# Optimization experiments

Hardware: AMD Instinct MI355X
Metric: run time of the kernel (lower is better)

## Reference

```python
import jax, jax.numpy as jnp
import numpy as np

N, C_IN, H, W = 1024, 22, 19, 19
C_TRUNK, HID, NHIST = 384, 128, 5
HIST_START = 9  # channels 9..13 hold move history planes


def setup_inputs() -> dict:
    key = jax.random.key(0)
    ks = jax.random.split(key, 8)
    return {
        "input_spatial": jax.random.uniform(ks[0], (N, C_IN, H, W), dtype=jnp.float32),
        "trunk_out": jax.random.normal(ks[1], (N, C_TRUNK, H, W), dtype=jnp.float32),
        "w_ih": jax.random.normal(ks[2], (4 * HID, C_TRUNK), dtype=jnp.float32) * 0.05,
        "w_hh": jax.random.normal(ks[3], (4 * HID, HID), dtype=jnp.float32) * 0.05,
        "b_ih": jax.random.normal(ks[4], (4 * HID,), dtype=jnp.float32) * 0.05,
        "b_hh": jax.random.normal(ks[5], (4 * HID,), dtype=jnp.float32) * 0.05,
        "w_proj": jax.random.normal(ks[6], (C_TRUNK, HID), dtype=jnp.float32) * 0.05,
        "b_proj": jax.random.normal(ks[7], (C_TRUNK,), dtype=jnp.float32) * 0.05,
    }


def reference(input_spatial, trunk_out, w_ih, w_hh, b_ih, b_hh, w_proj, b_proj):
    n, _, h, w = input_spatial.shape
    c_trunk = trunk_out.shape[1]
    # --- extract_move_coords (vectorized) ---
    planes = input_spatial[:, HIST_START:HIST_START + NHIST]          # N,5,H,W
    flat = planes.reshape(n, NHIST, h * w)                            # N,5,HW
    has_move = flat.sum(axis=-1) > 0.5                                # N,5 bool
    idx = jnp.argmax(flat, axis=-1)                                   # N,5 (== r*W+c; clamp(-1,min=0)==0 handled by mask)
    # --- gather trunk features at move coords, mask missing moves ---
    trunk_flat = trunk_out.reshape(n, c_trunk, h * w)                 # N,Ct,HW
    feats = jnp.take_along_axis(trunk_flat, idx[:, None, :], axis=2)  # N,Ct,5
    feats = feats.transpose(0, 2, 1) * has_move[..., None].astype(trunk_out.dtype)  # N,5,Ct
    seq = feats[:, ::-1, :]                                           # oldest -> newest
    # --- single-layer LSTM (torch gate order: i, f, g, o) ---
    def step(carry, x_t):
        h_t, c_t = carry
        g = x_t @ w_ih.T + h_t @ w_hh.T + b_ih + b_hh                 # N,4H
        i_g, f_g, g_g, o_g = jnp.split(g, 4, axis=-1)
        c_new = jax.nn.sigmoid(f_g) * c_t + jax.nn.sigmoid(i_g) * jnp.tanh(g_g)
        h_new = jax.nn.sigmoid(o_g) * jnp.tanh(c_new)
        return (h_new, c_new), None

    h0 = jnp.zeros((n, HID), dtype=seq.dtype)
    (h_final, _), _ = jax.lax.scan(step, (h0, h0), seq.transpose(1, 0, 2))
    out = h_final @ w_proj.T + b_proj                                 # N,Ct
    return out[:, :, None, None]                                      # N,Ct,1,1
```

## Files before the change

### kernel.cpp

```cpp
#include <hip/hip_runtime.h>
#include <hip/hip_bf16.h>
#include <float.h>

#define N_SAMP   1024
#define C_IN     22
#define HW       361
#define C_TRUNK  384
#define HID      128
#define NHIST    5
#define HIST_START 9
#define NGATE    512

typedef __attribute__((ext_vector_type(8))) short short8v;
typedef __attribute__((ext_vector_type(4))) float float4v;

static __device__ __forceinline__ ushort f2bf(float x) {
  unsigned int b = __float_as_uint(x);
  b += 0x7fffu + ((b >> 16) & 1u);
  return (ushort)(b >> 16);
}
static __device__ __forceinline__ float bf2f(ushort u) {
  return __uint_as_float(((unsigned int)u) << 16);
}

#define WIH_ELEMS   (NGATE * C_TRUNK)
#define WHH_ELEMS   (NGATE * HID)
#define WPROJ_ELEMS (C_TRUNK * HID)

__global__ __launch_bounds__(384) void prep_kernel(
    const float* __restrict__ inp,
    const float* __restrict__ w_ih,
    const float* __restrict__ w_hh,
    const float* __restrict__ w_proj,
    const float* __restrict__ trunk,
    ushort* __restrict__ w_ihb,
    ushort* __restrict__ w_hhb,
    ushort* __restrict__ w_projb,
    ushort* __restrict__ seq)
{
  const int n    = blockIdx.x;
  const int tid  = threadIdx.x;
  const int wave = tid >> 6;
  const int lane = tid & 63;
  __shared__ int   s_idx[NHIST];
  __shared__ float s_mov[NHIST];

  {
    const int g = n * 384 + tid;
    if (g < WIH_ELEMS) {
      w_ihb[g] = f2bf(w_ih[g]);
    } else if (g < WIH_ELEMS + WHH_ELEMS) {
      const int o = g - WIH_ELEMS;
      w_hhb[o] = f2bf(w_hh[o]);
    } else if (g < WIH_ELEMS + WHH_ELEMS + WPROJ_ELEMS) {
      const int o = g - WIH_ELEMS - WHH_ELEMS;
      w_projb[o] = f2bf(w_proj[o]);
    }
  }

  if (wave < NHIST) {
    const float* base = inp + ((size_t)n * C_IN + HIST_START + wave) * HW;
    float v = -FLT_MAX; int vi = 0; float sum = 0.f;
    #pragma unroll
    for (int r = 0; r < 6; ++r) {
      int i = lane + r * 64;
      if (i < HW) {
        float x = base[i];
        sum += x;
        if (x > v) { v = x; vi = i; }
      }
    }
    #pragma unroll
    for (int m = 1; m < 64; m <<= 1) {
      float v2 = __shfl_xor(v, m);
      int   i2 = __shfl_xor(vi, m);
      float s2 = __shfl_xor(sum, m);
      if (v2 > v || (v2 == v && i2 < vi)) { v = v2; vi = i2; }
      sum += s2;
    }
    if (lane == 0) {
      s_idx[wave] = vi;
      s_mov[wave] = (sum > 0.5f) ? 1.f : 0.f;
    }
  }
  __syncthreads();

  if (tid < 192) {
    const int c = tid;
    const int   i0 = s_idx[4], i1 = s_idx[3], i2 = s_idx[2],
                i3 = s_idx[1], i4 = s_idx[0];
    const float m0 = s_mov[4], m1 = s_mov[3], m2 = s_mov[2],
                m3 = s_mov[1], m4 = s_mov[0];

    const float* ta = trunk + ((size_t)n * C_TRUNK + c) * HW;
    const float* tb = ta + (size_t)192 * HW;
    float a0 = ta[i0], a1 = ta[i1], a2 = ta[i2], a3 = ta[i3], a4 = ta[i4];
    float b0 = tb[i0], b1 = tb[i1], b2 = tb[i2], b3 = tb[i3], b4 = tb[i4];

    ushort* so = seq + (size_t)n * NHIST * C_TRUNK + c;
    so[0 * C_TRUNK]       = f2bf(a0 * m0);
    so[1 * C_TRUNK]       = f2bf(a1 * m1);
    so[2 * C_TRUNK]       = f2bf(a2 * m2);
    so[3 * C_TRUNK]       = f2bf(a3 * m3);
    so[4 * C_TRUNK]       = f2bf(a4 * m4);
    so[0 * C_TRUNK + 192] = f2bf(b0 * m0);
    so[1 * C_TRUNK + 192] = f2bf(b1 * m1);
    so[2 * C_TRUNK + 192] = f2bf(b2 * m2);
    so[3 * C_TRUNK + 192] = f2bf(b3 * m3);
    so[4 * C_TRUNK + 192] = f2bf(b4 * m4);
  }
}

__global__ __launch_bounds__(256) void gates_kernel(
    const ushort* __restrict__ seq,
    const ushort* __restrict__ w_ihb,
    const float*  __restrict__ b_ih,
    const float*  __restrict__ b_hh,
    ushort* __restrict__ G)
{
  __shared__ ushort As[64][40];
  __shared__ ushort Bs[64][40];
  const int tid  = threadIdx.x;
  const int wv   = tid >> 6;
  const int lane = tid & 63;
  const int m0 = blockIdx.y * 64;
  const int j0 = blockIdx.x * 64;
  const int row_l = tid >> 2;
  const int koff  = (tid & 3) * 8;

  float4v acc0 = {0.f,0.f,0.f,0.f};
  float4v acc1 = {0.f,0.f,0.f,0.f};
  float4v acc2 = {0.f,0.f,0.f,0.f};
  float4v acc3 = {0.f,0.f,0.f,0.f};

  const int fr = lane & 15;
  const int fk = (lane >> 4) * 8;

  for (int k0 = 0; k0 < C_TRUNK; k0 += 32) {
    *(short8v*)&As[row_l][koff] =
        *(const short8v*)(seq + (size_t)(m0 + row_l) * C_TRUNK + k0 + koff);
    *(short8v*)&Bs[row_l][koff] =
        *(const short8v*)(w_ihb + (size_t)(j0 + row_l) * C_TRUNK + k0 + koff);
    __syncthreads();

    short8v af  = *(const short8v*)&As[wv * 16 + fr][fk];
    short8v bf0 = *(const short8v*)&Bs[ 0 + fr][fk];
    short8v bf1 = *(const short8v*)&Bs[16 + fr][fk];
    short8v bf2 = *(const short8v*)&Bs[32 + fr][fk];
    short8v bf3 = *(const short8v*)&Bs[48 + fr][fk];
    acc0 = __builtin_amdgcn_mfma_f32_16x16x32_bf16(af, bf0, acc0, 0, 0, 0);
    acc1 = __builtin_amdgcn_mfma_f32_16x16x32_bf16(af, bf1, acc1, 0, 0, 0);
    acc2 = __builtin_amdgcn_mfma_f32_16x16x32_bf16(af, bf2, acc2, 0, 0, 0);
    acc3 = __builtin_amdgcn_mfma_f32_16x16x32_bf16(af, bf3, acc3, 0, 0, 0);
    __syncthreads();
  }

  const int rbase = m0 + wv * 16 + (lane >> 4) * 4;
  #pragma unroll
  for (int j = 0; j < 4; ++j) {
    const float4v a = (j == 0) ? acc0 : (j == 1) ? acc1 : (j == 2) ? acc2 : acc3;
    const int cj = j0 + j * 16 + fr;
    const float bsum = b_ih[cj] + b_hh[cj];
    #pragma unroll
    for (int r = 0; r < 4; ++r)
      G[(size_t)(rbase + r) * NGATE + cj] = f2bf(a[r] + bsum);
  }
}

__global__ __launch_bounds__(512, 2) void lstm_kernel(
    const ushort* __restrict__ G,
    const ushort* __restrict__ w_hhb,
    const ushort* __restrict__ w_projb,
    const float*  __restrict__ b_proj,
    float* __restrict__ out)
{
  const int n0   = blockIdx.x * 4;
  const int tid  = threadIdx.x;
  const int wv   = tid >> 6;
  const int lane = tid & 63;
  const int fr   = lane & 15;
  const int fq   = lane >> 4;

  __shared__ ushort hswz[4][64][8];
  __shared__ float  glds[NGATE][4];

  ((ushort4*)hswz)[tid] = make_ushort4(0, 0, 0, 0);

  const int j0w = wv * 64;
  short8v bfrag[4][4];
  #pragma unroll
  for (int f = 0; f < 4; ++f)
    #pragma unroll
    for (int ks = 0; ks < 4; ++ks)
      bfrag[f][ks] = *(const short8v*)(
          w_hhb + (size_t)(j0w + f*16 + fr) * HID + ks*32 + fq*8);

  float4v gpre[NHIST][4];
  #pragma unroll
  for (int t = 0; t < NHIST; ++t)
    #pragma unroll
    for (int f = 0; f < 4; ++f) {
      float4v v = {0.f, 0.f, 0.f, 0.f};
      if (fq == 0) {
        const int col = j0w + f*16 + fr;
        #pragma unroll
        for (int r = 0; r < 4; ++r)
          v[r] = bf2f(G[((size_t)(n0 + r) * NHIST + t) * NGATE + col]);
      }
      gpre[t][f] = v;
    }

  float c4[4] = {0.f, 0.f, 0.f, 0.f};
  __syncthreads();

  #pragma unroll
  for (int t = 0; t < NHIST; ++t) {
    short8v af0 = *(const short8v*)&hswz[0][lane][0];
    short8v af1 = *(const short8v*)&hswz[1][lane][0];
    short8v af2 = *(const short8v*)&hswz[2][lane][0];
    short8v af3 = *(const short8v*)&hswz[3][lane][0];
    #pragma unroll
    for (int f = 0; f < 4; ++f) {
      float4v acc = gpre[t][f];
      acc = __builtin_amdgcn_mfma_f32_16x16x32_bf16(af0, bfrag[f][0], acc, 0, 0, 0);
      acc = __builtin_amdgcn_mfma_f32_16x16x32_bf16(af1, bfrag[f][1], acc, 0, 0, 0);
      acc = __builtin_amdgcn_mfma_f32_16x16x32_bf16(af2, bfrag[f][2], acc, 0, 0, 0);
      acc = __builtin_amdgcn_mfma_f32_16x16x32_bf16(af3, bfrag[f][3], acc, 0, 0, 0);
      if (fq == 0)
        *(float4v*)&glds[j0w + f*16 + fr][0] = acc;
    }
    __syncthreads();

    if (tid < HID) {
      const int j = tid;
      float4 iv = *(const float4*)&glds[      j][0];
      float4 fv = *(const float4*)&glds[128 + j][0];
      float4 gv = *(const float4*)&glds[256 + j][0];
      float4 ov = *(const float4*)&glds[384 + j][0];
      float ia[4] = {iv.x, iv.y, iv.z, iv.w};
      float fa[4] = {fv.x, fv.y, fv.z, fv.w};
      float ga[4] = {gv.x, gv.y, gv.z, gv.w};
      float oa[4] = {ov.x, ov.y, ov.z, ov.w};
      #pragma unroll
      for (int s = 0; s < 4; ++s) {
        float ig = 1.f / (1.f + __expf(-ia[s]));
        float fg = 1.f / (1.f + __expf(-fa[s]));
        float og = 1.f / (1.f + __expf(-oa[s]));
        c4[s] = fg * c4[s] + ig * tanhf(ga[s]);
        float h = og * tanhf(c4[s]);
        hswz[j >> 5][((j >> 3) & 3) * 16 + s][j & 7] = f2bf(h);
      }
    }
    __syncthreads();
  }

  const int j0p = wv * 48;
  short8v pfrag[3][4];
  #pragma unroll
  for (int f = 0; f < 3; ++f)
    #pragma unroll
    for (int ks = 0; ks < 4; ++ks)
      pfrag[f][ks] = *(const short8v*)(
          w_projb + (size_t)(j0p + f*16 + fr) * HID + ks*32 + fq*8);

  short8v hf0 = *(const short8v*)&hswz[0][lane][0];
  short8v hf1 = *(const short8v*)&hswz[1][lane][0];
  short8v hf2 = *(const short8v*)&hswz[2][lane][0];
  short8v hf3 = *(const short8v*)&hswz[3][lane][0];
  #pragma unroll
  for (int f = 0; f < 3; ++f) {
    const int col = j0p + f * 16 + fr;
    const float bp = b_proj[col];
    float4v acc = {bp, bp, bp, bp};
    acc = __builtin_amdgcn_mfma_f32_16x16x32_bf16(hf0, pfrag[f][0], acc, 0, 0, 0);
    acc = __builtin_amdgcn_mfma_f32_16x16x32_bf16(hf1, pfrag[f][1], acc, 0, 0, 0);
    acc = __builtin_amdgcn_mfma_f32_16x16x32_bf16(hf2, pfrag[f][2], acc, 0, 0, 0);
    acc = __builtin_amdgcn_mfma_f32_16x16x32_bf16(hf3, pfrag[f][3], acc, 0, 0, 0);
    if (fq == 0) {
      #pragma unroll
      for (int r = 0; r < 4; ++r)
        out[(size_t)(n0 + r) * C_TRUNK + col] = acc[r];
    }
  }
}

extern "C" void kernel_launch(void* const* d_in, const int* in_sizes, int n_in,
                              void* d_out, int out_size, void* d_ws, size_t ws_size,
                              hipStream_t stream) {
  const float* inp    = (const float*)d_in[0];
  const float* trunk  = (const float*)d_in[1];
  const float* w_ih   = (const float*)d_in[2];
  const float* w_hh   = (const float*)d_in[3];
  const float* b_ih   = (const float*)d_in[4];
  const float* b_hh   = (const float*)d_in[5];
  const float* w_proj = (const float*)d_in[6];
  const float* b_proj = (const float*)d_in[7];
  float* out = (float*)d_out;

  char* ws = (char*)d_ws;
  ushort* w_ihb   = (ushort*)ws;
  ushort* w_hhb   = (ushort*)(ws + 393216);
  ushort* w_projb = (ushort*)(ws + 524288);
  ushort* seq     = (ushort*)(ws + 622592);
  ushort* G       = (ushort*)(ws + 4554752);

  prep_kernel<<<N_SAMP, 384, 0, stream>>>(inp, w_ih, w_hh, w_proj, trunk,
                                          w_ihb, w_hhb, w_projb, seq);
  gates_kernel<<<dim3(NGATE / 64, (N_SAMP * NHIST) / 64), 256, 0, stream>>>(
      seq, w_ihb, b_ih, b_hh, G);
  lstm_kernel<<<N_SAMP / 4, 512, 0, stream>>>(G, w_hhb, w_projb, b_proj, out);
}
```

Measured before the change: 72.12 us.

## Fuse gather, input-gate GEMM and LSTM into one kernel per sample group

Splits weight conversion into its own small kernel, then fuses move extraction, trunk gather, the input-to-hidden GEMM and the LSTM recurrence into one kernel handling 4 samples per block. The gathered sequence stays in LDS and the gate pre-activations stay in registers, so the seq and G global round-trips and one launch go away. The cost is that the input GEMM now runs MFMA tiles with only 4 of 16 rows valid, which wastes matrix throughput. Each block also rereads the full w_ih from cache.

```diff
diff --git a/kernel.cpp b/kernel.cpp
--- a/kernel.cpp
+++ b/kernel.cpp
@@ -19,158 +19,40 @@
   b += 0x7fffu + ((b >> 16) & 1u);
   return (ushort)(b >> 16);
 }
-static __device__ __forceinline__ float bf2f(ushort u) {
-  return __uint_as_float(((unsigned int)u) << 16);
-}
 
 #define WIH_ELEMS   (NGATE * C_TRUNK)
 #define WHH_ELEMS   (NGATE * HID)
 #define WPROJ_ELEMS (C_TRUNK * HID)
-
-__global__ __launch_bounds__(384) void prep_kernel(
-    const float* __restrict__ inp,
+#define TOT_CVT     (WIH_ELEMS + WHH_ELEMS + WPROJ_ELEMS)
+
+__global__ __launch_bounds__(512) void precvt_kernel(
     const float* __restrict__ w_ih,
     const float* __restrict__ w_hh,
     const float* __restrict__ w_proj,
-    const float* __restrict__ trunk,
     ushort* __restrict__ w_ihb,
     ushort* __restrict__ w_hhb,
-    ushort* __restrict__ w_projb,
-    ushort* __restrict__ seq)
+    ushort* __restrict__ w_projb)
 {
-  const int n    = blockIdx.x;
-  const int tid  = threadIdx.x;
-  const int wave = tid >> 6;
-  const int lane = tid & 63;
-  __shared__ int   s_idx[NHIST];
-  __shared__ float s_mov[NHIST];
-
-  {
-    const int g = n * 384 + tid;
-    if (g < WIH_ELEMS) {
-      w_ihb[g] = f2bf(w_ih[g]);
-    } else if (g < WIH_ELEMS + WHH_ELEMS) {
-      const int o = g - WIH_ELEMS;
-      w_hhb[o] = f2bf(w_hh[o]);
-    } else if (g < WIH_ELEMS + WHH_ELEMS + WPROJ_ELEMS) {
-      const int o = g - WIH_ELEMS - WHH_ELEMS;
-      w_projb[o] = f2bf(w_proj[o]);
-    }
-  }
-
-  if (wave < NHIST) {
-    const float* base = inp + ((size_t)n * C_IN + HIST_START + wave) * HW;
-    float v = -FLT_MAX; int vi = 0; float sum = 0.f;
-    #pragma unroll
-    for (int r = 0; r < 6; ++r) {
-      int i = lane + r * 64;
-      if (i < HW) {
-        float x = base[i];
-        sum += x;
-        if (x > v) { v = x; vi = i; }
-      }
-    }
-    #pragma unroll
-    for (int m = 1; m < 64; m <<= 1) {
-      float v2 = __shfl_xor(v, m);
-      int   i2 = __shfl_xor(vi, m);
-      float s2 = __shfl_xor(sum, m);
-      if (v2 > v || (v2 == v && i2 < vi)) { v = v2; vi = i2; }
-      sum += s2;
-    }
-    if (lane == 0) {
-      s_idx[wave] = vi;
-      s_mov[wave] = (sum > 0.5f) ? 1.f : 0.f;
-    }
-  }
-  __syncthreads();
-
-  if (tid < 192) {
-    const int c = tid;
-    const int   i0 = s_idx[4], i1 = s_idx[3], i2 = s_idx[2],
-                i3 = s_idx[1], i4 = s_idx[0];
-    const float m0 = s_mov[4], m1 = s_mov[3], m2 = s_mov[2],
-                m3 = s_mov[1], m4 = s_mov[0];
-
-    const float* ta = trunk + ((size_t)n * C_TRUNK + c) * HW;
-    const float* tb = ta + (size_t)192 * HW;
-    float a0 = ta[i0], a1 = ta[i1], a2 = ta[i2], a3 = ta[i3], a4 = ta[i4];
-    float b0 = tb[i0], b1 = tb[i1], b2 = tb[i2], b3 = tb[i3], b4 = tb[i4];
-
-    ushort* so = seq + (size_t)n * NHIST * C_TRUNK + c;
-    so[0 * C_TRUNK]       = f2bf(a0 * m0);
-    so[1 * C_TRUNK]       = f2bf(a1 * m1);
-    so[2 * C_TRUNK]       = f2bf(a2 * m2);
-    so[3 * C_TRUNK]       = f2bf(a3 * m3);
-    so[4 * C_TRUNK]       = f2bf(a4 * m4);
-    so[0 * C_TRUNK + 192] = f2bf(b0 * m0);
-    so[1 * C_TRUNK + 192] = f2bf(b1 * m1);
-    so[2 * C_TRUNK + 192] = f2bf(b2 * m2);
-    so[3 * C_TRUNK + 192] = f2bf(b3 * m3);
-    so[4 * C_TRUNK + 192] = f2bf(b4 * m4);
-  }
-}
-
-__global__ __launch_bounds__(256) void gates_kernel(
-    const ushort* __restrict__ seq,
+  const int g = blockIdx.x * 512 + threadIdx.x;
+  if (g < WIH_ELEMS) {
+    w_ihb[g] = f2bf(w_ih[g]);
+  } else if (g < WIH_ELEMS + WHH_ELEMS) {
+    const int o = g - WIH_ELEMS;
+    w_hhb[o] = f2bf(w_hh[o]);
+  } else if (g < TOT_CVT) {
+    const int o = g - WIH_ELEMS - WHH_ELEMS;
+    w_projb[o] = f2bf(w_proj[o]);
+  }
+}
+
+__global__ __launch_bounds__(512) void mega_kernel(
+    const float*  __restrict__ inp,
+    const float*  __restrict__ trunk,
     const ushort* __restrict__ w_ihb,
+    const ushort* __restrict__ w_hhb,
+    const ushort* __restrict__ w_projb,
     const float*  __restrict__ b_ih,
     const float*  __restrict__ b_hh,
-    ushort* __restrict__ G)
-{
-  __shared__ ushort As[64][40];
-  __shared__ ushort Bs[64][40];
-  const int tid  = threadIdx.x;
-  const int wv   = tid >> 6;
-  const int lane = tid & 63;
-  const int m0 = blockIdx.y * 64;
-  const int j0 = blockIdx.x * 64;
-  const int row_l = tid >> 2;
-  const int koff  = (tid & 3) * 8;
-
-  float4v acc0 = {0.f,0.f,0.f,0.f};
-  float4v acc1 = {0.f,0.f,0.f,0.f};
-  float4v acc2 = {0.f,0.f,0.f,0.f};
-  float4v acc3 = {0.f,0.f,0.f,0.f};
-
-  const int fr = lane & 15;
-  const int fk = (lane >> 4) * 8;
-
-  for (int k0 = 0; k0 < C_TRUNK; k0 += 32) {
-    *(short8v*)&As[row_l][koff] =
-        *(const short8v*)(seq + (size_t)(m0 + row_l) * C_TRUNK + k0 + koff);
-    *(short8v*)&Bs[row_l][koff] =
-        *(const short8v*)(w_ihb + (size_t)(j0 + row_l) * C_TRUNK + k0 + koff);
-    __syncthreads();
-
-    short8v af  = *(const short8v*)&As[wv * 16 + fr][fk];
-    short8v bf0 = *(const short8v*)&Bs[ 0 + fr][fk];
-    short8v bf1 = *(const short8v*)&Bs[16 + fr][fk];
-    short8v bf2 = *(const short8v*)&Bs[32 + fr][fk];
-    short8v bf3 = *(const short8v*)&Bs[48 + fr][fk];
-    acc0 = __builtin_amdgcn_mfma_f32_16x16x32_bf16(af, bf0, acc0, 0, 0, 0);
-    acc1 = __builtin_amdgcn_mfma_f32_16x16x32_bf16(af, bf1, acc1, 0, 0, 0);
-    acc2 = __builtin_amdgcn_mfma_f32_16x16x32_bf16(af, bf2, acc2, 0, 0, 0);
-    acc3 = __builtin_amdgcn_mfma_f32_16x16x32_bf16(af, bf3, acc3, 0, 0, 0);
-    __syncthreads();
-  }
-
-  const int rbase = m0 + wv * 16 + (lane >> 4) * 4;
-  #pragma unroll
-  for (int j = 0; j < 4; ++j) {
-    const float4v a = (j == 0) ? acc0 : (j == 1) ? acc1 : (j == 2) ? acc2 : acc3;
-    const int cj = j0 + j * 16 + fr;
-    const float bsum = b_ih[cj] + b_hh[cj];
-    #pragma unroll
-    for (int r = 0; r < 4; ++r)
-      G[(size_t)(rbase + r) * NGATE + cj] = f2bf(a[r] + bsum);
-  }
-}
-
-__global__ __launch_bounds__(512, 2) void lstm_kernel(
-    const ushort* __restrict__ G,
-    const ushort* __restrict__ w_hhb,
-    const ushort* __restrict__ w_projb,
     const float*  __restrict__ b_proj,
     float* __restrict__ out)
 {
@@ -181,37 +63,101 @@
   const int fr   = lane & 15;
   const int fq   = lane >> 4;
 
+  __shared__ int    s_idx[4][NHIST];
+  __shared__ float  s_mov[4][NHIST];
+  __shared__ ushort seqs[4][NHIST][392];
   __shared__ ushort hswz[4][64][8];
   __shared__ float  glds[NGATE][4];
 
   ((ushort4*)hswz)[tid] = make_ushort4(0, 0, 0, 0);
 
+  for (int task = wv; task < 4 * NHIST; task += 8) {
+    const int s = task / NHIST, p = task - s * NHIST;
+    const float* base = inp + ((size_t)(n0 + s) * C_IN + HIST_START + p) * HW;
+    float v = -FLT_MAX; int vi = 0; float sum = 0.f;
+    #pragma unroll
+    for (int r6 = 0; r6 < 6; ++r6) {
+      int i = lane + r6 * 64;
+      if (i < HW) {
+        float x = base[i];
+        sum += x;
+        if (x > v) { v = x; vi = i; }
+      }
+    }
+    #pragma unroll
+    for (int m = 1; m < 64; m <<= 1) {
+      float v2 = __shfl_xor(v, m);
+      int   i2 = __shfl_xor(vi, m);
+      float s2 = __shfl_xor(sum, m);
+      if (v2 > v || (v2 == v && i2 < vi)) { v = v2; vi = i2; }
+      sum += s2;
+    }
+    if (lane == 0) {
+      s_idx[s][p] = vi;
+      s_mov[s][p] = (sum > 0.5f) ? 1.f : 0.f;
+    }
+  }
+  __syncthreads();
+
+  {
+    const int r0 = tid, r1 = tid + 512, r2 = tid + 1024;
+    const int sa = r0 / C_TRUNK, ca = r0 - sa * C_TRUNK;
+    const int sb = r1 / C_TRUNK, cb = r1 - sb * C_TRUNK;
+    const int sc = r2 / C_TRUNK, cc = r2 - sc * C_TRUNK;
+    const float* ta = trunk + ((size_t)(n0 + sa) * C_TRUNK + ca) * HW;
+    const float* tb = trunk + ((size_t)(n0 + sb) * C_TRUNK + cb) * HW;
+    const float* tc = trunk + ((size_t)(n0 + sc) * C_TRUNK + cc) * HW;
+    float xa[5], xb[5], xc[5];
+    #pragma unroll
+    for (int j = 0; j < 5; ++j) xa[j] = ta[s_idx[sa][j]];
+    #pragma unroll
+    for (int j = 0; j < 5; ++j) xb[j] = tb[s_idx[sb][j]];
+    #pragma unroll
+    for (int j = 0; j < 5; ++j) xc[j] = tc[s_idx[sc][j]];
+    #pragma unroll
+    for (int j = 0; j < 5; ++j) {
+      seqs[sa][4 - j][ca] = f2bf(xa[j] * s_mov[sa][j]);
+      seqs[sb][4 - j][cb] = f2bf(xb[j] * s_mov[sb][j]);
+      seqs[sc][4 - j][cc] = f2bf(xc[j] * s_mov[sc][j]);
+    }
+  }
+  __syncthreads();
+
   const int j0w = wv * 64;
+  float4v acc[NHIST][4];
+  #pragma unroll
+  for (int f = 0; f < 4; ++f) {
+    const int col = j0w + f * 16 + fr;
+    const float bsum = b_ih[col] + b_hh[col];
+    #pragma unroll
+    for (int t = 0; t < NHIST; ++t)
+      acc[t][f] = (float4v){bsum, bsum, bsum, bsum};
+  }
+  for (int ks = 0; ks < C_TRUNK / 32; ++ks) {
+    short8v bfv[4];
+    #pragma unroll
+    for (int f = 0; f < 4; ++f)
+      bfv[f] = *(const short8v*)(
+          w_ihb + (size_t)(j0w + f * 16 + fr) * C_TRUNK + ks * 32 + fq * 8);
+    #pragma unroll
+    for (int t = 0; t < NHIST; ++t) {
+      short8v af = {0, 0, 0, 0, 0, 0, 0, 0};
+      if (fr < 4) af = *(const short8v*)&seqs[fr][t][ks * 32 + fq * 8];
+      #pragma unroll
+      for (int f = 0; f < 4; ++f)
+        acc[t][f] = __builtin_amdgcn_mfma_f32_16x16x32_bf16(af, bfv[f], acc[t][f], 0, 0, 0);
+    }
+  }
+
   short8v bfrag[4][4];
   #pragma unroll
   for (int f = 0; f < 4; ++f)
     #pragma unroll
     for (int ks = 0; ks < 4; ++ks)
       bfrag[f][ks] = *(const short8v*)(
-          w_hhb + (size_t)(j0w + f*16 + fr) * HID + ks*32 + fq*8);
-
-  float4v gpre[NHIST][4];
-  #pragma unroll
-  for (int t = 0; t < NHIST; ++t)
-    #pragma unroll
-    for (int f = 0; f < 4; ++f) {
-      float4v v = {0.f, 0.f, 0.f, 0.f};
-      if (fq == 0) {
-        const int col = j0w + f*16 + fr;
-        #pragma unroll
-        for (int r = 0; r < 4; ++r)
-          v[r] = bf2f(G[((size_t)(n0 + r) * NHIST + t) * NGATE + col]);
-      }
-      gpre[t][f] = v;
-    }
+          w_hhb + (size_t)(j0w + f * 16 + fr) * HID + ks * 32 + fq * 8);
 
   float c4[4] = {0.f, 0.f, 0.f, 0.f};
-  __syncthreads();
 
   #pragma unroll
   for (int t = 0; t < NHIST; ++t) {
@@ -221,13 +167,13 @@
     short8v af3 = *(const short8v*)&hswz[3][lane][0];
     #pragma unroll
     for (int f = 0; f < 4; ++f) {
-      float4v acc = gpre[t][f];
-      acc = __builtin_amdgcn_mfma_f32_16x16x32_bf16(af0, bfrag[f][0], acc, 0, 0, 0);
-      acc = __builtin_amdgcn_mfma_f32_16x16x32_bf16(af1, bfrag[f][1], acc, 0, 0, 0);
-      acc = __builtin_amdgcn_mfma_f32_16x16x32_bf16(af2, bfrag[f][2], acc, 0, 0, 0);
-      acc = __builtin_amdgcn_mfma_f32_16x16x32_bf16(af3, bfrag[f][3], acc, 0, 0, 0);
+      float4v a = acc[t][f];
+      a = __builtin_amdgcn_mfma_f32_16x16x32_bf16(af0, bfrag[f][0], a, 0, 0, 0);
+      a = __builtin_amdgcn_mfma_f32_16x16x32_bf16(af1, bfrag[f][1], a, 0, 0, 0);
+      a = __builtin_amdgcn_mfma_f32_16x16x32_bf16(af2, bfrag[f][2], a, 0, 0, 0);
+      a = __builtin_amdgcn_mfma_f32_16x16x32_bf16(af3, bfrag[f][3], a, 0, 0, 0);
       if (fq == 0)
-        *(float4v*)&glds[j0w + f*16 + fr][0] = acc;
+        *(float4v*)&glds[j0w + f * 16 + fr][0] = a;
     }
     __syncthreads();
 
@@ -261,7 +207,7 @@
     #pragma unroll
     for (int ks = 0; ks < 4; ++ks)
       pfrag[f][ks] = *(const short8v*)(
-          w_projb + (size_t)(j0p + f*16 + fr) * HID + ks*32 + fq*8);
+          w_projb + (size_t)(j0p + f * 16 + fr) * HID + ks * 32 + fq * 8);
 
   short8v hf0 = *(const short8v*)&hswz[0][lane][0];
   short8v hf1 = *(const short8v*)&hswz[1][lane][0];
@@ -271,15 +217,15 @@
   for (int f = 0; f < 3; ++f) {
     const int col = j0p + f * 16 + fr;
     const float bp = b_proj[col];
-    float4v acc = {bp, bp, bp, bp};
-    acc = __builtin_amdgcn_mfma_f32_16x16x32_bf16(hf0, pfrag[f][0], acc, 0, 0, 0);
-    acc = __builtin_amdgcn_mfma_f32_16x16x32_bf16(hf1, pfrag[f][1], acc, 0, 0, 0);
-    acc = __builtin_amdgcn_mfma_f32_16x16x32_bf16(hf2, pfrag[f][2], acc, 0, 0, 0);
-    acc = __builtin_amdgcn_mfma_f32_16x16x32_bf16(hf3, pfrag[f][3], acc, 0, 0, 0);
+    float4v a = {bp, bp, bp, bp};
+    a = __builtin_amdgcn_mfma_f32_16x16x32_bf16(hf0, pfrag[f][0], a, 0, 0, 0);
+    a = __builtin_amdgcn_mfma_f32_16x16x32_bf16(hf1, pfrag[f][1], a, 0, 0, 0);
+    a = __builtin_amdgcn_mfma_f32_16x16x32_bf16(hf2, pfrag[f][2], a, 0, 0, 0);
+    a = __builtin_amdgcn_mfma_f32_16x16x32_bf16(hf3, pfrag[f][3], a, 0, 0, 0);
     if (fq == 0) {
       #pragma unroll
       for (int r = 0; r < 4; ++r)
-        out[(size_t)(n0 + r) * C_TRUNK + col] = acc[r];
+        out[(size_t)(n0 + r) * C_TRUNK + col] = a[r];
     }
   }
 }
@@ -301,12 +247,9 @@
   ushort* w_ihb   = (ushort*)ws;
   ushort* w_hhb   = (ushort*)(ws + 393216);
   ushort* w_projb = (ushort*)(ws + 524288);
-  ushort* seq     = (ushort*)(ws + 622592);
-  ushort* G       = (ushort*)(ws + 4554752);
-
-  prep_kernel<<<N_SAMP, 384, 0, stream>>>(inp, w_ih, w_hh, w_proj, trunk,
-                                          w_ihb, w_hhb, w_projb, seq);
-  gates_kernel<<<dim3(NGATE / 64, (N_SAMP * NHIST) / 64), 256, 0, stream>>>(
-      seq, w_ihb, b_ih, b_hh, G);
-  lstm_kernel<<<N_SAMP / 4, 512, 0, stream>>>(G, w_hhb, w_projb, b_proj, out);
-}
+
+  precvt_kernel<<<(TOT_CVT + 511) / 512, 512, 0, stream>>>(
+      w_ih, w_hh, w_proj, w_ihb, w_hhb, w_projb);
+  mega_kernel<<<N_SAMP / 4, 512, 0, stream>>>(
+      inp, trunk, w_ihb, w_hhb, w_projb, b_ih, b_hh, b_proj, out);
+}
```

Result: slower. 73.75 us (+2.3%).
